# Kernel optimization log

Hardware: AMD Instinct MI355X
Metric: run time of the kernel (lower is better)

Reference implementation:

```python
import jax, jax.numpy as jnp
import numpy as np

DIM = 2          # num_input_channels
NB = 8           # num_bins (normflows default)
TB = 3.0         # tail_bound
MINW = 1e-3; MINH = 1e-3; MIND = 1e-3
H = 128          # hidden_units
NL = 16          # flow_length
NBLK = 2         # hidden_layers (MADE residual blocks)
PM = 3 * NB - 1  # spline params per dim
DCONST = float(np.log(np.expm1(1.0 - MIND)))  # tail pad constant for derivatives
SQH = float(np.sqrt(H))
LU_EPS = 1e-3

# MADE masks for features=2: input degrees [1,2], all hidden degrees = 1
_M0 = np.zeros((H, DIM), np.float32); _M0[:, 0] = 1.0
_MF = np.zeros((DIM * PM, H), np.float32); _MF[PM:, :] = 1.0
M0 = jnp.asarray(_M0); MF = jnp.asarray(_MF)


def _mlp(x, w1, b1, w2, b2):
    return jax.nn.silu(x @ w1.T + b1) @ w2.T + b2


def _made(zin, W0, b0, Wres, bres, Wf, bf):
    h = zin @ (W0 * M0).T + b0
    for blk in range(NBLK):  # residual blocks (hidden masks all-ones for dim=2)
        t = jax.nn.relu(h)
        t = t @ Wres[blk, 0].T + bres[blk, 0]
        t = jax.nn.relu(t)
        t = t @ Wres[blk, 1].T + bres[blk, 1]
        h = h + t
    return (h @ (Wf * MF).T + bf).reshape(zin.shape[0], DIM, PM)


def _rqs_inverse(y, uw, uh, ud):
    # unconstrained rational-quadratic spline with linear tails, inverse direction
    widths = MINW + (1 - MINW * NB) * jax.nn.softmax(uw, -1)
    cw = jnp.concatenate([jnp.zeros_like(widths[..., :1]), jnp.cumsum(widths, -1)], -1)
    cw = (2 * TB * cw - TB).at[..., 0].set(-TB).at[..., -1].set(TB)
    widths = cw[..., 1:] - cw[..., :-1]
    heights = MINH + (1 - MINH * NB) * jax.nn.softmax(uh, -1)
    ch = jnp.concatenate([jnp.zeros_like(heights[..., :1]), jnp.cumsum(heights, -1)], -1)
    ch = (2 * TB * ch - TB).at[..., 0].set(-TB).at[..., -1].set(TB)
    heights = ch[..., 1:] - ch[..., :-1]
    pad = jnp.full(ud.shape[:-1] + (1,), DCONST, ud.dtype)
    d = MIND + jax.nn.softplus(jnp.concatenate([pad, ud, pad], -1))
    inside = (y >= -TB) & (y <= TB)
    yc = jnp.clip(y, -TB, TB)
    idx = jnp.clip(jnp.sum(yc[..., None] >= ch, -1) - 1, 0, NB - 1)[..., None]
    take = lambda a, i: jnp.take_along_axis(a, i, -1)[..., 0]
    yk = take(ch, idx); hk = take(heights, idx)
    xk = take(cw, idx); wk = take(widths, idx)
    dk = take(d, idx); dk1 = take(d, idx + 1)
    sk = hk / wk; dy = yc - yk; t2 = dk + dk1 - 2 * sk
    a = dy * t2 + hk * (sk - dk)
    b = hk * dk - dy * t2
    c = -sk * dy
    disc = jnp.maximum(b * b - 4 * a * c, 0.0)
    theta = 2 * c / (-b - jnp.sqrt(disc))
    xo = theta * wk + xk
    om = 1 - theta
    denom = sk + t2 * theta * om
    dnum = (sk * sk) * (dk1 * theta * theta + 2 * sk * theta * om + dk * om * om)
    ld_fwd = jnp.log(dnum) - 2 * jnp.log(denom)
    return jnp.where(inside, xo, y), jnp.where(inside, -ld_fwd, 0.0)


def _flow_forward(z_0, x, sigma, n1_w1, n1_b1, n1_w2, n1_b2, n2_w1, n2_b1, n2_w2, n2_b2,
                  made_W0, made_b0, made_Wres, made_bres, made_Wf, made_bf,
                  lu_lower, lu_upper, lu_diag, lu_bias, perms):
    tcond = _mlp(sigma, n1_w1, n1_b1, n1_w2, n1_b2)
    z = _mlp(jnp.concatenate([z_0, x], -1), n2_w1, n2_b1, n2_w2, n2_b2) + tcond
    ld_tot = jnp.zeros(z.shape[0], z.dtype)
    for i in range(NL):
        # AR RQ-spline flow: flow.forward() == sequential inverse of MADE spline
        y = z
        out = jnp.zeros_like(y)
        ldp = jnp.zeros_like(y)
        for _ in range(DIM):
            p = _made(out, made_W0[i], made_b0[i], made_Wres[i], made_bres[i], made_Wf[i], made_bf[i])
            out, ldp = _rqs_inverse(y, p[..., :NB] / SQH, p[..., NB:2 * NB] / SQH, p[..., 2 * NB:])
        ld_tot = ld_tot + ldp.sum(-1)
        # LULinearPermute.forward == LU-linear inverse then permutation inverse
        diag = jax.nn.softplus(lu_diag[i]) + LU_EPS
        Lm = jnp.eye(DIM, dtype=z.dtype).at[1, 0].set(lu_lower[i])
        Um = jnp.diag(diag).at[0, 1].set(lu_upper[i])
        Wm = Lm @ Um
        z = (out - lu_bias[i]) @ jnp.linalg.inv(Wm).T
        ld_tot = ld_tot - jnp.sum(jnp.log(diag))
        z = z[:, perms[i]]
    return z, ld_tot


def setup_inputs() -> dict:
    key = jax.random.key(0)
    ks = jax.random.split(key, 20)
    B = 262144
    f = jnp.float32
    rn = lambda k, s, sc=1.0: jax.random.normal(k, s, dtype=f) * sc
    inp = {}
    inp["z_0"] = rn(ks[0], (B, DIM))
    inp["x"] = rn(ks[1], (B, DIM))
    inp["sigma"] = jax.random.uniform(ks[2], (B, 1), dtype=f)
    inp["n1_w1"] = rn(ks[3], (32, 1), 0.5); inp["n1_b1"] = jnp.zeros((32,), f)
    inp["n1_w2"] = rn(ks[4], (DIM, 32), 0.2); inp["n1_b2"] = jnp.zeros((DIM,), f)
    inp["n2_w1"] = rn(ks[5], (32, 2 * DIM), 0.5); inp["n2_b1"] = jnp.zeros((32,), f)
    inp["n2_w2"] = rn(ks[6], (DIM, 32), 0.2); inp["n2_b2"] = jnp.zeros((DIM,), f)
    inp["made_W0"] = rn(ks[7], (NL, H, DIM), 0.3)
    inp["made_b0"] = rn(ks[8], (NL, H), 0.1)
    inp["made_Wres"] = rn(ks[9], (NL, NBLK, 2, H, H), 0.05)
    inp["made_bres"] = rn(ks[10], (NL, NBLK, 2, H), 0.05)
    inp["made_Wf"] = rn(ks[11], (NL, DIM * PM, H), 0.05)
    inp["made_bf"] = rn(ks[12], (NL, DIM * PM), 0.05)
    inp["lu_lower"] = rn(ks[13], (NL,), 0.3)
    inp["lu_upper"] = rn(ks[14], (NL,), 0.3)
    inp["lu_diag"] = rn(ks[15], (NL, DIM), 0.3) + 0.5413  # softplus^-1(1)
    inp["lu_bias"] = rn(ks[16], (NL, DIM), 0.1)
    inp["perms"] = jnp.asarray(np.stack([[1, 0] if i % 2 else [0, 1] for i in range(NL)]).astype(np.int32))
    return inp


def reference(z_0, x, sigma, n1_w1, n1_b1, n1_w2, n1_b2, n2_w1, n2_b1, n2_w2, n2_b2,
              made_W0, made_b0, made_Wres, made_bres, made_Wf, made_bf,
              lu_lower, lu_upper, lu_diag, lu_bias, perms):
    return _flow_forward(z_0, x, sigma, n1_w1, n1_b1, n1_w2, n1_b2, n2_w1, n2_b1, n2_w2, n2_b2,
                         made_W0, made_b0, made_Wres, made_bres, made_Wf, made_bf,
                         lu_lower, lu_upper, lu_diag, lu_bias, perms)
```

## Files before the change

### kernel.cpp

```cpp
#include <hip/hip_runtime.h>
#include <math.h>

#define NBATCH 262144
#define INVSQH 0.08838834764831845f

#define NPT   2048
#define NGRID 1920
#define TROW  24

#define WT_OFF   0
#define WFT_OFF  4194304
#define WS0_OFF  4456448
#define TAB_OFF  4464640
#define REC_OFF  7610368
#define LDC_OFF  7612928

__device__ __forceinline__ float fastrcp(float x) {
#if __has_builtin(__builtin_amdgcn_rcpf)
    return __builtin_amdgcn_rcpf(x);
#else
    return 1.f / x;
#endif
}
__device__ __forceinline__ float fastdiv(float a, float b) { return a * fastrcp(b); }
__device__ __forceinline__ float fastsqrt(float x) {
#if __has_builtin(__builtin_amdgcn_sqrtf)
    return __builtin_amdgcn_sqrtf(x);
#else
    return sqrtf(x);
#endif
}

__device__ __forceinline__ float softplusf(float x) {
    return (x > 15.f) ? x : __logf(1.f + __expf(x));
}

__device__ __forceinline__ float gridval(int i) {
    float v = -56.8f + i * 0.25f;
    if (i >= 192)  v = -8.8f + (i - 192) * 0.0125f;
    if (i >= 1600) v = 9.05f + (i - 1600) * 0.25f;
    if (i >= 1792) v = 58.5f + (i - 1792) * 0.01f;
    return v;
}
__device__ __forceinline__ int cnt_grid_le_fast(float x) {
    if (x < -56.8f) return 0;
    if (x < -8.8f)  return min((int)floorf((x + 56.8f) * 4.0f) + 1, 192);
    if (x < 9.05f)  return 192 + min((int)floorf((x + 8.8f) * 80.0f) + 1, 1408);
    if (x < 58.5f)  return 1600 + min((int)floorf((x - 9.05f) * 4.0f) + 1, 192);
    return 1792 + min((int)floorf((x - 58.5f) * 100.0f) + 1, 128);
}

__device__ __forceinline__ void rqs_solve(float y, float yc, float yk, float hk, float xk,
                                          float wk, float dk, float dk1,
                                          float& xout, float& ldout)
{
    float sk = fastdiv(hk, wk);
    float dy = yc - yk;
    float t2 = dk + dk1 - 2.f * sk;
    float av = dy * t2 + hk * (sk - dk);
    float bv = hk * dk - dy * t2;
    float cv = -sk * dy;
    float disc = fmaxf(bv * bv - 4.f * av * cv, 0.f);
    float theta = 2.f * cv * fastrcp(-bv - fastsqrt(disc));
    float xo = fmaf(theta, wk, xk);
    float om = 1.f - theta;
    float denom = fmaf(t2, theta * om, sk);
    float dnum = sk * sk * (dk1 * theta * theta + 2.f * sk * theta * om + dk * om * om);
    float rden = fastrcp(denom);
    float ldf = __logf(dnum * rden * rden);
    bool inside = (y >= -3.f) && (y <= 3.f);
    xout  = inside ? xo : y;
    ldout = inside ? -ldf : 0.f;
}

__device__ __forceinline__ void knots_from_p(const float* __restrict__ p,
                                             float* __restrict__ cw,
                                             float* __restrict__ ch,
                                             float* __restrict__ d)
{
    float uw[8], uh[8];
#pragma unroll
    for (int j = 0; j < 8; ++j) uw[j] = p[j] * INVSQH;
#pragma unroll
    for (int j = 0; j < 8; ++j) uh[j] = p[8 + j] * INVSQH;
    float mw = uw[0], mh = uh[0];
#pragma unroll
    for (int j = 1; j < 8; ++j) { mw = fmaxf(mw, uw[j]); mh = fmaxf(mh, uh[j]); }
    float ew[8], eh[8], sw = 0.f, sh = 0.f;
#pragma unroll
    for (int j = 0; j < 8; ++j) {
        ew[j] = __expf(uw[j] - mw); sw += ew[j];
        eh[j] = __expf(uh[j] - mh); sh += eh[j];
    }
    float isw = 0.992f * fastrcp(sw), ish = 0.992f * fastrcp(sh);
    cw[0] = -3.f; ch[0] = -3.f;
    float aw = 0.f, ah = 0.f;
#pragma unroll
    for (int j = 0; j < 8; ++j) {
        aw += 0.001f + ew[j] * isw;
        ah += 0.001f + eh[j] * ish;
        cw[j + 1] = 6.f * aw - 3.f;
        ch[j + 1] = 6.f * ah - 3.f;
    }
    cw[8] = 3.f; ch[8] = 3.f;
    d[0] = 1.f; d[8] = 1.f;
#pragma unroll
    for (int j = 0; j < 7; ++j) d[j + 1] = 0.001f + softplusf(p[16 + j]);
}

__device__ __forceinline__ void rqs_from_knots(float y, const float* __restrict__ cw,
                                               const float* __restrict__ ch,
                                               const float* __restrict__ d,
                                               float& xout, float& ldout)
{
    float yc = fminf(fmaxf(y, -3.f), 3.f);
    float yk = ch[0], hk = ch[1] - ch[0], xk = cw[0], wk = cw[1] - cw[0];
    float dk = d[0], dk1 = d[1];
#pragma unroll
    for (int j = 1; j < 8; ++j) {
        bool cge = (yc >= ch[j]);
        yk  = cge ? ch[j] : yk;
        hk  = cge ? (ch[j + 1] - ch[j]) : hk;
        xk  = cge ? cw[j] : xk;
        wk  = cge ? (cw[j + 1] - cw[j]) : wk;
        dk  = cge ? d[j] : dk;
        dk1 = cge ? d[j + 1] : dk1;
    }
    rqs_solve(y, yc, yk, hk, xk, wk, dk, dk1, xout, ldout);
}

__device__ __forceinline__ void rqs_knots(float y, const float* __restrict__ rec,
                                          float& xout, float& ldout)
{
    rqs_from_knots(y, rec, rec + 9, rec + 18, xout, ldout);
}

extern "C" __global__ __launch_bounds__(256)
void nsf_prep(const float* __restrict__ Wresg, const float* __restrict__ Wfg,
              const float* __restrict__ W0g,  const float* __restrict__ b0g,
              const float* __restrict__ bfg,
              const float* __restrict__ lulg, const float* __restrict__ luug,
              const float* __restrict__ ludg, const float* __restrict__ lubg,
              const int* __restrict__ permsg, char* __restrict__ ws)
{
    const int b = blockIdx.x, tid = threadIdx.x;
    float* WT  = (float*)(ws + WT_OFF);
    float* WFT = (float*)(ws + WFT_OFF);
    float* ws0 = (float*)(ws + WS0_OFF);

    if (b < 256) {
        __shared__ float T[64][65];
        const int mat = b >> 2, tr = (b >> 1) & 1, tc = b & 1;
        const float* src = Wresg + mat * 16384;
        float* dst = WT + mat * 16384;
        const int r = tid >> 2, q = tid & 3;
#pragma unroll
        for (int i = 0; i < 4; ++i) {
            int c4 = q * 4 + i;
            float4 v = *(const float4*)(src + (tr * 64 + r) * 128 + tc * 64 + c4 * 4);
            T[r][c4 * 4 + 0] = v.x; T[r][c4 * 4 + 1] = v.y;
            T[r][c4 * 4 + 2] = v.z; T[r][c4 * 4 + 3] = v.w;
        }
        __syncthreads();
        const int kk = tid >> 2;
#pragma unroll
        for (int i = 0; i < 4; ++i) {
            int u4 = q * 4 + i;
            float4 v;
            v.x = T[u4 * 4 + 0][kk]; v.y = T[u4 * 4 + 1][kk];
            v.z = T[u4 * 4 + 2][kk]; v.w = T[u4 * 4 + 3][kk];
            *(float4*)(dst + (tc * 64 + kk) * 128 + tr * 64 + u4 * 4) = v;
        }
        return;
    }

    const int L = b - 256;
    for (int e = tid; e < 4096; e += 256) {
        int k = e >> 5, o = e & 31;
        WFT[L * 4096 + e] = (o < 23) ? Wfg[(L * 46 + 23 + o) * 128 + k] : 0.f;
    }
    if (tid < 128) ws0[L * 128 + tid] = W0g[L * 256 + 2 * tid];

    if (tid == 0) {
        float* rec = (float*)(ws + REC_OFF) + L * 40;
        const float* p = bfg + L * 46;
        for (int half = 0; half < 2; ++half) {
            float u[8], m = -1e30f;
            for (int j = 0; j < 8; ++j) { u[j] = p[half * 8 + j] * INVSQH; m = fmaxf(m, u[j]); }
            float e[8], ssum = 0.f;
            for (int j = 0; j < 8; ++j) { e[j] = expf(u[j] - m); ssum += e[j]; }
            float cum = 0.f;
            rec[half * 9 + 0] = -3.f;
            for (int j = 0; j < 8; ++j) {
                cum += 0.001f + 0.992f * e[j] / ssum;
                rec[half * 9 + 1 + j] = 6.f * cum - 3.f;
            }
            rec[half * 9 + 8] = 3.f;
        }
        rec[18] = 1.f; rec[26] = 1.f;
        for (int j = 0; j < 7; ++j) {
            float x = p[16 + j];
            rec[19 + j] = 0.001f + ((x > 15.f) ? x : log1pf(expf(x)));
        }
        float x0 = ludg[2 * L], x1 = ludg[2 * L + 1];
        float dg0 = 0.001f + ((x0 > 15.f) ? x0 : log1pf(expf(x0)));
        float dg1 = 0.001f + ((x1 > 15.f) ? x1 : log1pf(expf(x1)));
        float ll = lulg[L], uu = luug[L];
        float det = dg0 * dg1;
        float c00 = (ll * uu + dg1) / det, c01 = -uu / det;
        float c10 = -ll / dg1, c11 = 1.f / dg1;
        int pa = permsg[2 * L], pb2 = permsg[2 * L + 1];
        rec[27] = pa ? c10 : c00;  rec[28] = pa ? c11 : c01;
        rec[29] = pb2 ? c10 : c00; rec[30] = pb2 ? c11 : c01;
        rec[31] = lubg[2 * L];     rec[32] = lubg[2 * L + 1];
    }
    if (L == 0 && tid == 32) {
        float ssum = 0.f;
        for (int l2 = 0; l2 < 16; ++l2) {
            float x0 = ludg[2 * l2], x1 = ludg[2 * l2 + 1];
            float dg0 = 0.001f + ((x0 > 15.f) ? x0 : log1pf(expf(x0)));
            float dg1 = 0.001f + ((x1 > 15.f) ? x1 : log1pf(expf(x1)));
            ssum += logf(dg0) + logf(dg1);
        }
        *(float*)(ws + LDC_OFF) = ssum;
    }
}

extern "C" __global__ __launch_bounds__(256, 4)
void nsf_eval(const float* __restrict__ bresg, const float* __restrict__ b0g,
              const float* __restrict__ bfg, char* __restrict__ ws)
{
    __shared__ float R[128 * 36];
    __shared__ float p1sh[32 * 24];
    const int tid = threadIdx.x;
    const int lane = tid & 63, w = tid >> 6;
    const int u0 = w * 32 + (lane & 7) * 4;
    const int p0 = (lane >> 3) * 4;
    const int L = blockIdx.x >> 6;
    const int pb = (blockIdx.x & 63) << 5;

    const float* WT  = (const float*)(ws + WT_OFF);
    const float* WFT = (const float*)(ws + WFT_OFF);
    const float* ws0 = (const float*)(ws + WS0_OFF);
    float* tab = (float*)(ws + TAB_OFF);

    float H[4][4];
    {
        float sp[4] = {gridval(pb + p0), gridval(pb + p0 + 1),
                       gridval(pb + p0 + 2), gridval(pb + p0 + 3)};
        float4 a0 = *(const float4*)(ws0 + L * 128 + u0);
        float4 c0 = *(const float4*)(b0g + L * 128 + u0);
        float aj[4] = {a0.x, a0.y, a0.z, a0.w};
        float cj[4] = {c0.x, c0.y, c0.z, c0.w};
#pragma unroll
        for (int j = 0; j < 4; ++j) {
#pragma unroll
            for (int p = 0; p < 4; ++p) H[j][p] = fmaf(aj[j], sp[p], cj[j]);
            float4 v = {fmaxf(H[j][0], 0.f), fmaxf(H[j][1], 0.f),
                        fmaxf(H[j][2], 0.f), fmaxf(H[j][3], 0.f)};
            *(float4*)(&R[(u0 + j) * 36 + p0]) = v;
        }
    }
    __syncthreads();

#pragma unroll 1
    for (int st = 0; st < 4; ++st) {
        const float* Wst = WT + (L * 4 + st) * 16384;
        const float* bb  = bresg + (L * 4 + st) * 128;
        float acc[4][4];
        {
            float4 b0v = *(const float4*)(bb + u0);
            float bj[4] = {b0v.x, b0v.y, b0v.z, b0v.w};
#pragma unroll
            for (int j = 0; j < 4; ++j)
#pragma unroll
                for (int p = 0; p < 4; ++p) acc[j][p] = bj[j];
        }
#pragma unroll 4
        for (int k = 0; k < 128; ++k) {
            float4 w0 = *(const float4*)(Wst + k * 128 + u0);
            float4 r  = *(const float4*)(&R[k * 36 + p0]);
            float wj[4] = {w0.x, w0.y, w0.z, w0.w};
            float rp[4] = {r.x, r.y, r.z, r.w};
#pragma unroll
            for (int j = 0; j < 4; ++j)
#pragma unroll
                for (int p = 0; p < 4; ++p)
                    acc[j][p] = fmaf(wj[j], rp[p], acc[j][p]);
        }
        if (st == 1 || st == 3) {
#pragma unroll
            for (int j = 0; j < 4; ++j)
#pragma unroll
                for (int p = 0; p < 4; ++p) H[j][p] += acc[j][p];
        }
        __syncthreads();
#pragma unroll
        for (int j = 0; j < 4; ++j) {
            float4 v;
            if (st == 0 || st == 2) {
                v = (float4){fmaxf(acc[j][0], 0.f), fmaxf(acc[j][1], 0.f),
                             fmaxf(acc[j][2], 0.f), fmaxf(acc[j][3], 0.f)};
            } else if (st == 1) {
                v = (float4){fmaxf(H[j][0], 0.f), fmaxf(H[j][1], 0.f),
                             fmaxf(H[j][2], 0.f), fmaxf(H[j][3], 0.f)};
            } else {
                v = (float4){H[j][0], H[j][1], H[j][2], H[j][3]};
            }
            *(float4*)(&R[(u0 + j) * 36 + p0]) = v;
        }
        __syncthreads();
    }

    {
        const int o = tid & 31, pg4 = tid >> 5;
        float pacc[4] = {0.f, 0.f, 0.f, 0.f};
#pragma unroll 4
        for (int k = 0; k < 128; ++k) {
            float wf = WFT[(L * 128 + k) * 32 + o];
            float4 ra = *(const float4*)(&R[k * 36 + pg4 * 4]);
            pacc[0] = fmaf(wf, ra.x, pacc[0]);
            pacc[1] = fmaf(wf, ra.y, pacc[1]);
            pacc[2] = fmaf(wf, ra.z, pacc[2]);
            pacc[3] = fmaf(wf, ra.w, pacc[3]);
        }
        if (o < 23) {
            float bias = bfg[L * 46 + 23 + o];
#pragma unroll
            for (int p = 0; p < 4; ++p)
                p1sh[(pg4 * 4 + p) * 24 + o] = pacc[p] + bias;
        }
    }
    __syncthreads();

    if (tid < 32) {
        float pp[23];
#pragma unroll
        for (int j = 0; j < 23; ++j) pp[j] = p1sh[tid * 24 + j];
        float cw[9], ch[9], d[9];
        knots_from_p(pp, cw, ch, d);
        float out[24];
#pragma unroll
        for (int i = 0; i < 8; ++i) out[i] = cw[i + 1];
#pragma unroll
        for (int i = 0; i < 8; ++i) out[8 + i] = ch[i + 1];
#pragma unroll
        for (int i = 0; i < 7; ++i) out[16 + i] = d[i + 1];
        out[23] = gridval(pb + tid);
        float4* dst = (float4*)(tab + (L * NPT + pb + tid) * TROW);
#pragma unroll
        for (int i = 0; i < 6; ++i)
            dst[i] = ((const float4*)out)[i];
    }
}

extern "C" __global__ __launch_bounds__(256, 4)
void nsf_main(const float* __restrict__ z0g, const float* __restrict__ xg,
              const float* __restrict__ sgg,
              const float* __restrict__ n1w1, const float* __restrict__ n1b1,
              const float* __restrict__ n1w2, const float* __restrict__ n1b2,
              const float* __restrict__ n2w1, const float* __restrict__ n2b1,
              const float* __restrict__ n2w2, const float* __restrict__ n2b2,
              const char* __restrict__ ws, float* __restrict__ outg)
{
    __shared__ float recs_s[16 * 40];

    const float* tab  = (const float*)(ws + TAB_OFF);
    const float* recg = (const float*)(ws + REC_OFF);

    const int tid = threadIdx.x;
    const int s = blockIdx.x * 256 + tid;

    for (int i = tid; i < 640; i += 256) recs_s[i] = recg[i];
    __syncthreads();

    float zz0, zz1, ld = 0.f;
    {
        float za = z0g[2 * s], zb = z0g[2 * s + 1];
        float xa = xg[2 * s],  xb = xg[2 * s + 1];
        float sg = sgg[s];
        float t0 = n1b2[0], t1 = n1b2[1];
#pragma unroll
        for (int m = 0; m < 32; ++m) {
            float hm = fmaf(sg, n1w1[m], n1b1[m]);
            hm = hm * fastrcp(1.f + __expf(-hm));
            t0 = fmaf(hm, n1w2[m], t0);
            t1 = fmaf(hm, n1w2[32 + m], t1);
        }
        float u0 = n2b2[0], u1 = n2b2[1];
#pragma unroll
        for (int m = 0; m < 32; ++m) {
            float hm = za * n2w1[4 * m] + zb * n2w1[4 * m + 1]
                     + xa * n2w1[4 * m + 2] + xb * n2w1[4 * m + 3] + n2b1[m];
            hm = hm * fastrcp(1.f + __expf(-hm));
            u0 = fmaf(hm, n2w2[m], u0);
            u1 = fmaf(hm, n2w2[32 + m], u1);
        }
        zz0 = u0 + t0; zz1 = u1 + t1;
    }

    for (int L = 0; L < 16; ++L) {
        const float* rec = recs_s + L * 40;
        float out0, ldp0;
        rqs_knots(zz0, rec, out0, ldp0);

        int pos = min(max(cnt_grid_le_fast(out0) - 1, 0), NGRID - 2);

        const float4* r4 = (const float4*)(tab + (L * NPT + pos) * TROW);
        float4 q0[6], q1[6];
#pragma unroll
        for (int i = 0; i < 6; ++i) { q0[i] = r4[i]; q1[i] = r4[i + 6]; }

        float e0 = q0[5].w, e1 = q1[5].w;
        float de = e1 - e0;
        float tt = (de > 1e-9f) ? (out0 - e0) * fastrcp(de) : 0.f;

        float cw[9], ch[9], d[9];
        cw[0] = -3.f; ch[0] = -3.f; d[0] = 1.f; d[8] = 1.f;
#pragma unroll
        for (int i = 0; i < 2; ++i) {
            cw[4 * i + 1] = fmaf(tt, q1[i].x - q0[i].x, q0[i].x);
            cw[4 * i + 2] = fmaf(tt, q1[i].y - q0[i].y, q0[i].y);
            cw[4 * i + 3] = fmaf(tt, q1[i].z - q0[i].z, q0[i].z);
            cw[4 * i + 4] = fmaf(tt, q1[i].w - q0[i].w, q0[i].w);
            ch[4 * i + 1] = fmaf(tt, q1[i + 2].x - q0[i + 2].x, q0[i + 2].x);
            ch[4 * i + 2] = fmaf(tt, q1[i + 2].y - q0[i + 2].y, q0[i + 2].y);
            ch[4 * i + 3] = fmaf(tt, q1[i + 2].z - q0[i + 2].z, q0[i + 2].z);
            ch[4 * i + 4] = fmaf(tt, q1[i + 2].w - q0[i + 2].w, q0[i + 2].w);
        }
        d[1] = fmaf(tt, q1[4].x - q0[4].x, q0[4].x);
        d[2] = fmaf(tt, q1[4].y - q0[4].y, q0[4].y);
        d[3] = fmaf(tt, q1[4].z - q0[4].z, q0[4].z);
        d[4] = fmaf(tt, q1[4].w - q0[4].w, q0[4].w);
        d[5] = fmaf(tt, q1[5].x - q0[5].x, q0[5].x);
        d[6] = fmaf(tt, q1[5].y - q0[5].y, q0[5].y);
        d[7] = fmaf(tt, q1[5].z - q0[5].z, q0[5].z);

        float out1, ldp1;
        rqs_from_knots(zz1, cw, ch, d, out1, ldp1);
        ld += ldp0 + ldp1;

        float v0 = out0 - rec[31], v1 = out1 - rec[32];
        zz0 = fmaf(v0, rec[27], v1 * rec[28]);
        zz1 = fmaf(v0, rec[29], v1 * rec[30]);
    }

    float ldc = *(const float*)(ws + LDC_OFF);
    outg[2 * s] = zz0;
    outg[2 * s + 1] = zz1;
    outg[2 * NBATCH + s] = ld - ldc;
}

extern "C" void kernel_launch(void* const* d_in, const int* in_sizes, int n_in,
                              void* d_out, int out_size, void* d_ws, size_t ws_size,
                              hipStream_t stream)
{
    const float* z0g  = (const float*)d_in[0];
    const float* xg   = (const float*)d_in[1];
    const float* sgg  = (const float*)d_in[2];
    const float* n1w1 = (const float*)d_in[3];
    const float* n1b1 = (const float*)d_in[4];
    const float* n1w2 = (const float*)d_in[5];
    const float* n1b2 = (const float*)d_in[6];
    const float* n2w1 = (const float*)d_in[7];
    const float* n2b1 = (const float*)d_in[8];
    const float* n2w2 = (const float*)d_in[9];
    const float* n2b2 = (const float*)d_in[10];
    const float* W0g  = (const float*)d_in[11];
    const float* b0g  = (const float*)d_in[12];
    const float* Wres = (const float*)d_in[13];
    const float* bres = (const float*)d_in[14];
    const float* Wfg  = (const float*)d_in[15];
    const float* bfg  = (const float*)d_in[16];
    const float* lul  = (const float*)d_in[17];
    const float* luu  = (const float*)d_in[18];
    const float* lud  = (const float*)d_in[19];
    const float* lub  = (const float*)d_in[20];
    const int*   perms= (const int*)d_in[21];
    float* outg = (float*)d_out;
    char* ws = (char*)d_ws;

    nsf_prep<<<272, 256, 0, stream>>>(Wres, Wfg, W0g, b0g, bfg, lul, luu, lud, lub, perms, ws);
    nsf_eval<<<1024, 256, 0, stream>>>(bres, b0g, bfg, ws);
    nsf_main<<<NBATCH / 256, 256, 0, stream>>>(z0g, xg, sgg,
                                               n1w1, n1b1, n1w2, n1b2,
                                               n2w1, n2b1, n2w2, n2b2,
                                               ws, outg);
}
```

Baseline: 271.2 us.

## Drop prep kernel: read weights untransposed in eval, build records in main

Removes the nsf_prep launch that transposed the residual and final-layer weights and built per-layer spline records in workspace. nsf_eval now reads the original row-major Wres with float4 loads along k per output unit, and reads Wf rows directly. nsf_main computes the per-layer records and the log-det constant into shared memory in every block. This saves one launch and the transpose traffic, but the eval weight loads become strided across lanes, and every main block repeats the small record computation.

```diff
diff --git a/kernel.cpp b/kernel.cpp
--- a/kernel.cpp
+++ b/kernel.cpp
@@ -8,12 +8,7 @@
 #define NGRID 1920
 #define TROW  24
 
-#define WT_OFF   0
-#define WFT_OFF  4194304
-#define WS0_OFF  4456448
-#define TAB_OFF  4464640
-#define REC_OFF  7610368
-#define LDC_OFF  7612928
+#define TAB_OFF 0
 
 __device__ __forceinline__ float fastrcp(float x) {
 #if __has_builtin(__builtin_amdgcn_rcpf)
@@ -129,60 +124,178 @@
     rqs_solve(y, yc, yk, hk, xk, wk, dk, dk1, xout, ldout);
 }
 
-__device__ __forceinline__ void rqs_knots(float y, const float* __restrict__ rec,
-                                          float& xout, float& ldout)
-{
-    rqs_from_knots(y, rec, rec + 9, rec + 18, xout, ldout);
-}
-
-extern "C" __global__ __launch_bounds__(256)
-void nsf_prep(const float* __restrict__ Wresg, const float* __restrict__ Wfg,
+extern "C" __global__ __launch_bounds__(256, 4)
+void nsf_eval(const float* __restrict__ Wresg, const float* __restrict__ bresg,
               const float* __restrict__ W0g,  const float* __restrict__ b0g,
+              const float* __restrict__ Wfg,  const float* __restrict__ bfg,
+              char* __restrict__ ws)
+{
+    __shared__ float R[128 * 36];
+    __shared__ float p1sh[32 * 24];
+    const int tid = threadIdx.x;
+    const int lane = tid & 63, w = tid >> 6;
+    const int u0 = w * 32 + (lane & 7) * 4;
+    const int p0 = (lane >> 3) * 4;
+    const int L = blockIdx.x >> 6;
+    const int pb = (blockIdx.x & 63) << 5;
+
+    float* tab = (float*)(ws + TAB_OFF);
+
+    float H[4][4];
+    {
+        float sp[4] = {gridval(pb + p0), gridval(pb + p0 + 1),
+                       gridval(pb + p0 + 2), gridval(pb + p0 + 3)};
+        float aj[4], cj[4];
+#pragma unroll
+        for (int j = 0; j < 4; ++j) {
+            aj[j] = W0g[L * 256 + 2 * (u0 + j)];
+            cj[j] = b0g[L * 128 + u0 + j];
+        }
+#pragma unroll
+        for (int j = 0; j < 4; ++j) {
+#pragma unroll
+            for (int p = 0; p < 4; ++p) H[j][p] = fmaf(aj[j], sp[p], cj[j]);
+            float4 v = {fmaxf(H[j][0], 0.f), fmaxf(H[j][1], 0.f),
+                        fmaxf(H[j][2], 0.f), fmaxf(H[j][3], 0.f)};
+            *(float4*)(&R[(u0 + j) * 36 + p0]) = v;
+        }
+    }
+    __syncthreads();
+
+#pragma unroll 1
+    for (int st = 0; st < 4; ++st) {
+        const float* Wst = Wresg + (L * 4 + st) * 16384;
+        const float* bb  = bresg + (L * 4 + st) * 128;
+        float acc[4][4];
+        {
+            float4 b0v = *(const float4*)(bb + u0);
+            float bj[4] = {b0v.x, b0v.y, b0v.z, b0v.w};
+#pragma unroll
+            for (int j = 0; j < 4; ++j)
+#pragma unroll
+                for (int p = 0; p < 4; ++p) acc[j][p] = bj[j];
+        }
+#pragma unroll 2
+        for (int k4 = 0; k4 < 32; ++k4) {
+            float4 w4[4], r4[4];
+#pragma unroll
+            for (int j = 0; j < 4; ++j)
+                w4[j] = *(const float4*)(Wst + (u0 + j) * 128 + k4 * 4);
+#pragma unroll
+            for (int kk = 0; kk < 4; ++kk)
+                r4[kk] = *(const float4*)(&R[(k4 * 4 + kk) * 36 + p0]);
+            float wjk[4][4] = {
+                {w4[0].x, w4[0].y, w4[0].z, w4[0].w},
+                {w4[1].x, w4[1].y, w4[1].z, w4[1].w},
+                {w4[2].x, w4[2].y, w4[2].z, w4[2].w},
+                {w4[3].x, w4[3].y, w4[3].z, w4[3].w}};
+            float rkp[4][4] = {
+                {r4[0].x, r4[0].y, r4[0].z, r4[0].w},
+                {r4[1].x, r4[1].y, r4[1].z, r4[1].w},
+                {r4[2].x, r4[2].y, r4[2].z, r4[2].w},
+                {r4[3].x, r4[3].y, r4[3].z, r4[3].w}};
+#pragma unroll
+            for (int kk = 0; kk < 4; ++kk)
+#pragma unroll
+                for (int j = 0; j < 4; ++j)
+#pragma unroll
+                    for (int p = 0; p < 4; ++p)
+                        acc[j][p] = fmaf(wjk[j][kk], rkp[kk][p], acc[j][p]);
+        }
+        if (st == 1 || st == 3) {
+#pragma unroll
+            for (int j = 0; j < 4; ++j)
+#pragma unroll
+                for (int p = 0; p < 4; ++p) H[j][p] += acc[j][p];
+        }
+        __syncthreads();
+#pragma unroll
+        for (int j = 0; j < 4; ++j) {
+            float4 v;
+            if (st == 0 || st == 2) {
+                v = (float4){fmaxf(acc[j][0], 0.f), fmaxf(acc[j][1], 0.f),
+                             fmaxf(acc[j][2], 0.f), fmaxf(acc[j][3], 0.f)};
+            } else if (st == 1) {
+                v = (float4){fmaxf(H[j][0], 0.f), fmaxf(H[j][1], 0.f),
+                             fmaxf(H[j][2], 0.f), fmaxf(H[j][3], 0.f)};
+            } else {
+                v = (float4){H[j][0], H[j][1], H[j][2], H[j][3]};
+            }
+            *(float4*)(&R[(u0 + j) * 36 + p0]) = v;
+        }
+        __syncthreads();
+    }
+
+    {
+        const int o = tid & 31, pg4 = tid >> 5;
+        if (o < 23) {
+            const float* wrow = Wfg + (L * 46 + 23 + o) * 128;
+            float pacc[4] = {0.f, 0.f, 0.f, 0.f};
+#pragma unroll 2
+            for (int k4 = 0; k4 < 32; ++k4) {
+                float4 wv = *(const float4*)(wrow + k4 * 4);
+                float wk4[4] = {wv.x, wv.y, wv.z, wv.w};
+#pragma unroll
+                for (int kk = 0; kk < 4; ++kk) {
+                    float4 ra = *(const float4*)(&R[(k4 * 4 + kk) * 36 + pg4 * 4]);
+                    pacc[0] = fmaf(wk4[kk], ra.x, pacc[0]);
+                    pacc[1] = fmaf(wk4[kk], ra.y, pacc[1]);
+                    pacc[2] = fmaf(wk4[kk], ra.z, pacc[2]);
+                    pacc[3] = fmaf(wk4[kk], ra.w, pacc[3]);
+                }
+            }
+            float bias = bfg[L * 46 + 23 + o];
+#pragma unroll
+            for (int p = 0; p < 4; ++p)
+                p1sh[(pg4 * 4 + p) * 24 + o] = pacc[p] + bias;
+        }
+    }
+    __syncthreads();
+
+    if (tid < 32) {
+        float pp[23];
+#pragma unroll
+        for (int j = 0; j < 23; ++j) pp[j] = p1sh[tid * 24 + j];
+        float cw[9], ch[9], d[9];
+        knots_from_p(pp, cw, ch, d);
+        float out[24];
+#pragma unroll
+        for (int i = 0; i < 8; ++i) out[i] = cw[i + 1];
+#pragma unroll
+        for (int i = 0; i < 8; ++i) out[8 + i] = ch[i + 1];
+#pragma unroll
+        for (int i = 0; i < 7; ++i) out[16 + i] = d[i + 1];
+        out[23] = gridval(pb + tid);
+        float4* dst = (float4*)(tab + (L * NPT + pb + tid) * TROW);
+#pragma unroll
+        for (int i = 0; i < 6; ++i)
+            dst[i] = ((const float4*)out)[i];
+    }
+}
+
+extern "C" __global__ __launch_bounds__(256, 4)
+void nsf_main(const float* __restrict__ z0g, const float* __restrict__ xg,
+              const float* __restrict__ sgg,
+              const float* __restrict__ n1w1, const float* __restrict__ n1b1,
+              const float* __restrict__ n1w2, const float* __restrict__ n1b2,
+              const float* __restrict__ n2w1, const float* __restrict__ n2b1,
+              const float* __restrict__ n2w2, const float* __restrict__ n2b2,
               const float* __restrict__ bfg,
               const float* __restrict__ lulg, const float* __restrict__ luug,
               const float* __restrict__ ludg, const float* __restrict__ lubg,
-              const int* __restrict__ permsg, char* __restrict__ ws)
-{
-    const int b = blockIdx.x, tid = threadIdx.x;
-    float* WT  = (float*)(ws + WT_OFF);
-    float* WFT = (float*)(ws + WFT_OFF);
-    float* ws0 = (float*)(ws + WS0_OFF);
-
-    if (b < 256) {
-        __shared__ float T[64][65];
-        const int mat = b >> 2, tr = (b >> 1) & 1, tc = b & 1;
-        const float* src = Wresg + mat * 16384;
-        float* dst = WT + mat * 16384;
-        const int r = tid >> 2, q = tid & 3;
-#pragma unroll
-        for (int i = 0; i < 4; ++i) {
-            int c4 = q * 4 + i;
-            float4 v = *(const float4*)(src + (tr * 64 + r) * 128 + tc * 64 + c4 * 4);
-            T[r][c4 * 4 + 0] = v.x; T[r][c4 * 4 + 1] = v.y;
-            T[r][c4 * 4 + 2] = v.z; T[r][c4 * 4 + 3] = v.w;
-        }
-        __syncthreads();
-        const int kk = tid >> 2;
-#pragma unroll
-        for (int i = 0; i < 4; ++i) {
-            int u4 = q * 4 + i;
-            float4 v;
-            v.x = T[u4 * 4 + 0][kk]; v.y = T[u4 * 4 + 1][kk];
-            v.z = T[u4 * 4 + 2][kk]; v.w = T[u4 * 4 + 3][kk];
-            *(float4*)(dst + (tc * 64 + kk) * 128 + tr * 64 + u4 * 4) = v;
-        }
-        return;
-    }
-
-    const int L = b - 256;
-    for (int e = tid; e < 4096; e += 256) {
-        int k = e >> 5, o = e & 31;
-        WFT[L * 4096 + e] = (o < 23) ? Wfg[(L * 46 + 23 + o) * 128 + k] : 0.f;
-    }
-    if (tid < 128) ws0[L * 128 + tid] = W0g[L * 256 + 2 * tid];
-
-    if (tid == 0) {
-        float* rec = (float*)(ws + REC_OFF) + L * 40;
+              const int* __restrict__ permsg,
+              const char* __restrict__ ws, float* __restrict__ outg)
+{
+    __shared__ float recs_s[16 * 40];
+    __shared__ float ldc_s;
+
+    const float* tab = (const float*)(ws + TAB_OFF);
+    const int tid = threadIdx.x;
+    const int s = blockIdx.x * 256 + tid;
+
+    if (tid < 16) {
+        const int L = tid;
+        float* rec = recs_s + L * 40;
         const float* p = bfg + L * 46;
         for (int half = 0; half < 2; ++half) {
             float u[8], m = -1e30f;
@@ -213,8 +326,7 @@
         rec[27] = pa ? c10 : c00;  rec[28] = pa ? c11 : c01;
         rec[29] = pb2 ? c10 : c00; rec[30] = pb2 ? c11 : c01;
         rec[31] = lubg[2 * L];     rec[32] = lubg[2 * L + 1];
-    }
-    if (L == 0 && tid == 32) {
+    } else if (tid == 16) {
         float ssum = 0.f;
         for (int l2 = 0; l2 < 16; ++l2) {
             float x0 = ludg[2 * l2], x1 = ludg[2 * l2 + 1];
@@ -222,157 +334,8 @@
             float dg1 = 0.001f + ((x1 > 15.f) ? x1 : log1pf(expf(x1)));
             ssum += logf(dg0) + logf(dg1);
         }
-        *(float*)(ws + LDC_OFF) = ssum;
-    }
-}
-
-extern "C" __global__ __launch_bounds__(256, 4)
-void nsf_eval(const float* __restrict__ bresg, const float* __restrict__ b0g,
-              const float* __restrict__ bfg, char* __restrict__ ws)
-{
-    __shared__ float R[128 * 36];
-    __shared__ float p1sh[32 * 24];
-    const int tid = threadIdx.x;
-    const int lane = tid & 63, w = tid >> 6;
-    const int u0 = w * 32 + (lane & 7) * 4;
-    const int p0 = (lane >> 3) * 4;
-    const int L = blockIdx.x >> 6;
-    const int pb = (blockIdx.x & 63) << 5;
-
-    const float* WT  = (const float*)(ws + WT_OFF);
-    const float* WFT = (const float*)(ws + WFT_OFF);
-    const float* ws0 = (const float*)(ws + WS0_OFF);
-    float* tab = (float*)(ws + TAB_OFF);
-
-    float H[4][4];
-    {
-        float sp[4] = {gridval(pb + p0), gridval(pb + p0 + 1),
-                       gridval(pb + p0 + 2), gridval(pb + p0 + 3)};
-        float4 a0 = *(const float4*)(ws0 + L * 128 + u0);
-        float4 c0 = *(const float4*)(b0g + L * 128 + u0);
-        float aj[4] = {a0.x, a0.y, a0.z, a0.w};
-        float cj[4] = {c0.x, c0.y, c0.z, c0.w};
-#pragma unroll
-        for (int j = 0; j < 4; ++j) {
-#pragma unroll
-            for (int p = 0; p < 4; ++p) H[j][p] = fmaf(aj[j], sp[p], cj[j]);
-            float4 v = {fmaxf(H[j][0], 0.f), fmaxf(H[j][1], 0.f),
-                        fmaxf(H[j][2], 0.f), fmaxf(H[j][3], 0.f)};
-            *(float4*)(&R[(u0 + j) * 36 + p0]) = v;
-        }
-    }
-    __syncthreads();
-
-#pragma unroll 1
-    for (int st = 0; st < 4; ++st) {
-        const float* Wst = WT + (L * 4 + st) * 16384;
-        const float* bb  = bresg + (L * 4 + st) * 128;
-        float acc[4][4];
-        {
-            float4 b0v = *(const float4*)(bb + u0);
-            float bj[4] = {b0v.x, b0v.y, b0v.z, b0v.w};
-#pragma unroll
-            for (int j = 0; j < 4; ++j)
-#pragma unroll
-                for (int p = 0; p < 4; ++p) acc[j][p] = bj[j];
-        }
-#pragma unroll 4
-        for (int k = 0; k < 128; ++k) {
-            float4 w0 = *(const float4*)(Wst + k * 128 + u0);
-            float4 r  = *(const float4*)(&R[k * 36 + p0]);
-            float wj[4] = {w0.x, w0.y, w0.z, w0.w};
-            float rp[4] = {r.x, r.y, r.z, r.w};
-#pragma unroll
-            for (int j = 0; j < 4; ++j)
-#pragma unroll
-                for (int p = 0; p < 4; ++p)
-                    acc[j][p] = fmaf(wj[j], rp[p], acc[j][p]);
-        }
-        if (st == 1 || st == 3) {
-#pragma unroll
-            for (int j = 0; j < 4; ++j)
-#pragma unroll
-                for (int p = 0; p < 4; ++p) H[j][p] += acc[j][p];
-        }
-        __syncthreads();
-#pragma unroll
-        for (int j = 0; j < 4; ++j) {
-            float4 v;
-            if (st == 0 || st == 2) {
-                v = (float4){fmaxf(acc[j][0], 0.f), fmaxf(acc[j][1], 0.f),
-                             fmaxf(acc[j][2], 0.f), fmaxf(acc[j][3], 0.f)};
-            } else if (st == 1) {
-                v = (float4){fmaxf(H[j][0], 0.f), fmaxf(H[j][1], 0.f),
-                             fmaxf(H[j][2], 0.f), fmaxf(H[j][3], 0.f)};
-            } else {
-                v = (float4){H[j][0], H[j][1], H[j][2], H[j][3]};
-            }
-            *(float4*)(&R[(u0 + j) * 36 + p0]) = v;
-        }
-        __syncthreads();
-    }
-
-    {
-        const int o = tid & 31, pg4 = tid >> 5;
-        float pacc[4] = {0.f, 0.f, 0.f, 0.f};
-#pragma unroll 4
-        for (int k = 0; k < 128; ++k) {
-            float wf = WFT[(L * 128 + k) * 32 + o];
-            float4 ra = *(const float4*)(&R[k * 36 + pg4 * 4]);
-            pacc[0] = fmaf(wf, ra.x, pacc[0]);
-            pacc[1] = fmaf(wf, ra.y, pacc[1]);
-            pacc[2] = fmaf(wf, ra.z, pacc[2]);
-            pacc[3] = fmaf(wf, ra.w, pacc[3]);
-        }
-        if (o < 23) {
-            float bias = bfg[L * 46 + 23 + o];
-#pragma unroll
-            for (int p = 0; p < 4; ++p)
-                p1sh[(pg4 * 4 + p) * 24 + o] = pacc[p] + bias;
-        }
-    }
-    __syncthreads();
-
-    if (tid < 32) {
-        float pp[23];
-#pragma unroll
-        for (int j = 0; j < 23; ++j) pp[j] = p1sh[tid * 24 + j];
-        float cw[9], ch[9], d[9];
-        knots_from_p(pp, cw, ch, d);
-        float out[24];
-#pragma unroll
-        for (int i = 0; i < 8; ++i) out[i] = cw[i + 1];
-#pragma unroll
-        for (int i = 0; i < 8; ++i) out[8 + i] = ch[i + 1];
-#pragma unroll
-        for (int i = 0; i < 7; ++i) out[16 + i] = d[i + 1];
-        out[23] = gridval(pb + tid);
-        float4* dst = (float4*)(tab + (L * NPT + pb + tid) * TROW);
-#pragma unroll
-        for (int i = 0; i < 6; ++i)
-            dst[i] = ((const float4*)out)[i];
-    }
-}
-
-extern "C" __global__ __launch_bounds__(256, 4)
-void nsf_main(const float* __restrict__ z0g, const float* __restrict__ xg,
-              const float* __restrict__ sgg,
-              const float* __restrict__ n1w1, const float* __restrict__ n1b1,
-              const float* __restrict__ n1w2, const float* __restrict__ n1b2,
-              const float* __restrict__ n2w1, const float* __restrict__ n2b1,
-              const float* __restrict__ n2w2, const float* __restrict__ n2b2,
-              const char* __restrict__ ws, float* __restrict__ outg)
-{
-    __shared__ float recs_s[16 * 40];
-
-    const float* tab  = (const float*)(ws + TAB_OFF);
-    const float* recg = (const float*)(ws + REC_OFF);
-
-    const int tid = threadIdx.x;
-    const int s = blockIdx.x * 256 + tid;
-
-    for (int i = tid; i < 640; i += 256) recs_s[i] = recg[i];
-    __syncthreads();
+        ldc_s = ssum;
+    }
 
     float zz0, zz1, ld = 0.f;
     {
@@ -398,11 +361,12 @@
         }
         zz0 = u0 + t0; zz1 = u1 + t1;
     }
+    __syncthreads();
 
     for (int L = 0; L < 16; ++L) {
         const float* rec = recs_s + L * 40;
         float out0, ldp0;
-        rqs_knots(zz0, rec, out0, ldp0);
+        rqs_from_knots(zz0, rec, rec + 9, rec + 18, out0, ldp0);
 
         int pos = min(max(cnt_grid_le_fast(out0) - 1, 0), NGRID - 2);
 
@@ -445,10 +409,9 @@
         zz1 = fmaf(v0, rec[29], v1 * rec[30]);
     }
 
-    float ldc = *(const float*)(ws + LDC_OFF);
     outg[2 * s] = zz0;
     outg[2 * s + 1] = zz1;
-    outg[2 * NBATCH + s] = ld - ldc;
+    outg[2 * NBATCH + s] = ld - ldc_s;
 }
 
 extern "C" void kernel_launch(void* const* d_in, const int* in_sizes, int n_in,
@@ -480,10 +443,10 @@
     float* outg = (float*)d_out;
     char* ws = (char*)d_ws;
 
-    nsf_prep<<<272, 256, 0, stream>>>(Wres, Wfg, W0g, b0g, bfg, lul, luu, lud, lub, perms, ws);
-    nsf_eval<<<1024, 256, 0, stream>>>(bres, b0g, bfg, ws);
+    nsf_eval<<<1024, 256, 0, stream>>>(Wres, bres, W0g, b0g, Wfg, bfg, ws);
     nsf_main<<<NBATCH / 256, 256, 0, stream>>>(z0g, xg, sgg,
                                                n1w1, n1b1, n1w2, n1b2,
                                                n2w1, n2b1, n2w2, n2b2,
+                                               bfg, lul, luu, lud, lub, perms,
                                                ws, outg);
 }
```

Result: slower. 426.1 us (+57.1%).
